# Performance work log

Hardware: AMD Instinct MI355X
Metric: run time of the kernel (lower is better)

Reference implementation:

```python
import jax, jax.numpy as jnp
import numpy as np

B, P, NOBJ = 16, 19248, 32
NUM_CLASSES = 81  # 80 foreground + background (code uses num_classes+1 w/o focal loss)
POS_TH, NEG_TH = 0.5, 0.4
VAR0, VAR1 = 0.1, 0.2  # standard SSD encode variances
NEGPOS_RATIO = 3


def setup_inputs() -> dict:
    key = jax.random.key(0)
    k1, k2, k3, k4, k5 = jax.random.split(key, 5)
    loc_data = jax.random.normal(k1, (B, P, 4), jnp.float32)
    conf_data = jax.random.normal(k2, (B, P, NUM_CLASSES), jnp.float32)
    # priors in (cx, cy, w, h), normalized coords
    pc = jax.random.uniform(k3, (P, 2), jnp.float32, 0.05, 0.95)
    pw = jax.random.uniform(jax.random.fold_in(k3, 1), (P, 2), jnp.float32, 0.05, 0.4)
    priors = jnp.concatenate([pc, pw], -1)
    # gt boxes in point form (xmin, ymin, xmax, ymax)
    gc = jax.random.uniform(k4, (B, NOBJ, 2), jnp.float32, 0.2, 0.8)
    gw = jax.random.uniform(jax.random.fold_in(k4, 1), (B, NOBJ, 2), jnp.float32, 0.05, 0.3)
    gt_boxes = jnp.concatenate([gc - gw / 2, gc + gw / 2], -1)
    gt_labels = jax.random.randint(k5, (B, NOBJ), 0, NUM_CLASSES - 1)  # 0..79
    return {"loc_data": loc_data, "conf_data": conf_data, "priors": priors,
            "gt_boxes": gt_boxes, "gt_labels": gt_labels}


def _point_form(p):
    # (cx,cy,w,h) -> (xmin,ymin,xmax,ymax)
    return jnp.concatenate([p[..., :2] - p[..., 2:] / 2, p[..., :2] + p[..., 2:] / 2], -1)


def _jaccard(a, b):
    # a: [N,4], b: [P,4] point form -> IoU [N,P]
    lt = jnp.maximum(a[:, None, :2], b[None, :, :2])
    rb = jnp.minimum(a[:, None, 2:], b[None, :, 2:])
    wh = jnp.clip(rb - lt, 0.0)
    inter = wh[..., 0] * wh[..., 1]
    area_a = (a[:, 2] - a[:, 0]) * (a[:, 3] - a[:, 1])
    area_b = (b[:, 2] - b[:, 0]) * (b[:, 3] - b[:, 1])
    return inter / (area_a[:, None] + area_b[None, :] - inter)


def _match_one(gt, labels, priors_pf, priors):
    # SSD match: per-prior best gt + force each gt's best prior to be positive
    ov = _jaccard(gt, priors_pf)                 # [N,P]
    best_prior_idx = jnp.argmax(ov, axis=1)      # [N]
    best_truth_ov = jnp.max(ov, axis=0)          # [P]
    best_truth_idx = jnp.argmax(ov, axis=0)      # [P]
    best_truth_ov = best_truth_ov.at[best_prior_idx].set(2.0)
    best_truth_idx = best_truth_idx.at[best_prior_idx].set(jnp.arange(gt.shape[0]))
    matched = gt[best_truth_idx]                 # [P,4] point form
    conf = labels[best_truth_idx] + 1
    conf = jnp.where(best_truth_ov < POS_TH, -1, conf)   # neutral band
    conf = jnp.where(best_truth_ov < NEG_TH, 0, conf)    # background
    # encode offsets with variances
    m_cxcy = (matched[:, :2] + matched[:, 2:]) / 2
    m_wh = matched[:, 2:] - matched[:, :2]
    g_cxcy = (m_cxcy - priors[:, :2]) / (VAR0 * priors[:, 2:])
    g_wh = jnp.log(m_wh / priors[:, 2:]) / VAR1
    return jnp.concatenate([g_cxcy, g_wh], -1), conf


def reference(loc_data, conf_data, priors, gt_boxes, gt_labels):
    priors_pf = _point_form(priors)
    loc_t, conf_t = jax.vmap(lambda g, l: _match_one(g, l, priors_pf, priors))(gt_boxes, gt_labels)
    loc_t = jax.lax.stop_gradient(loc_t)
    pos = conf_t > 0                                   # [B,P]
    n_pos = pos.sum(axis=1)                            # [B]
    N = jnp.maximum(pos.sum(), 1).astype(loc_data.dtype)
    # localization: smooth L1 over positives
    d = loc_data - loc_t
    ad = jnp.abs(d)
    sl1 = jnp.where(ad < 1.0, 0.5 * d * d, ad - 0.5)
    loss_l = jnp.sum(sl1 * pos[..., None])
    # confidence: hard negative mining at 3:1
    logp = jax.nn.log_softmax(conf_data, axis=-1)      # [B,P,C]
    ct = jnp.maximum(conf_t, 0)
    nll = -jnp.take_along_axis(logp, ct[..., None], axis=-1)[..., 0]  # [B,P]
    mine = jnp.where(pos | (conf_t < 0), 0.0, nll)     # exclude pos & neutral from mining
    rank = jnp.argsort(jnp.argsort(-mine, axis=1), axis=1)
    num_neg = jnp.minimum(NEGPOS_RATIO * n_pos, P - 1)
    neg = (rank < num_neg[:, None]) & (conf_t == 0)
    loss_c = jnp.sum(nll * (pos | neg))
    return jnp.stack([loss_l, loss_c]) / N
```

## Files before the change

### kernel.cpp

```cpp
#include <hip/hip_runtime.h>
#include <cstdint>
#include <cstddef>

#define BB 16
#define PP 19248
#define NOBJ 32
#define NCLS 81
#define POS_TH 0.5f
#define NEG_TH 0.4f
#define VAR0 0.1f
#define VAR1 0.2f
#define NEGPOS 3

#define MTB 256
#define NMB ((PP + MTB - 1) / MTB)
#define MAINB 1024
#define ROWS_PB 64
#define NSLOT ((PP + ROWS_PB - 1) / ROWS_PB)
#define ST 1024

#define HSHIFT 19
#define HSIZE 8192
#define HPT (HSIZE / ST)
#define CAP HSIZE

__global__ __launch_bounds__(MTB) void k_match(const float* __restrict__ priors,
                                               const float* __restrict__ gt_boxes,
                                               unsigned long long* __restrict__ gkey,
                                               float* __restrict__ bto,
                                               int* __restrict__ bti) {
    const int b = blockIdx.y;
    const int p = blockIdx.x * MTB + threadIdx.x;
    const int wid = threadIdx.x >> 6, lane = threadIdx.x & 63;
    __shared__ float4 sg[NOBJ];
    __shared__ unsigned long long wkey[4][NOBJ];
    if (threadIdx.x < NOBJ) sg[threadIdx.x] = ((const float4*)gt_boxes)[b * NOBJ + threadIdx.x];
    __syncthreads();

    const bool valid = p < PP;
    float px1 = 0.f, py1 = 0.f, px2 = 0.f, py2 = 0.f, parea = 0.f;
    if (valid) {
        float4 pr = ((const float4*)priors)[p];
        float hw = pr.z / 2.0f, hh = pr.w / 2.0f;
        px1 = pr.x - hw; py1 = pr.y - hh; px2 = pr.x + hw; py2 = pr.y + hh;
        parea = (px2 - px1) * (py2 - py1);
    }

    float best = -1.0f;
    int bn = 0;
    for (int n = 0; n < NOBJ; ++n) {
        float4 g = sg[n];
        float iou = -1.0f;
        if (valid) {
            {
#pragma clang fp contract(off)
                float ix1 = fmaxf(g.x, px1), iy1 = fmaxf(g.y, py1);
                float ix2 = fminf(g.z, px2), iy2 = fminf(g.w, py2);
                float iw = fmaxf(ix2 - ix1, 0.0f), ih = fmaxf(iy2 - iy1, 0.0f);
                float inter = iw * ih;
                float garea = (g.z - g.x) * (g.w - g.y);
                iou = inter / (garea + parea - inter);
            }
        }
        if (iou > best) { best = iou; bn = n; }

        float m = iou;
        m = fmaxf(m, __shfl_xor(m, 1, 64));
        m = fmaxf(m, __shfl_xor(m, 2, 64));
        m = fmaxf(m, __shfl_xor(m, 4, 64));
        m = fmaxf(m, __shfl_xor(m, 8, 64));
        m = fmaxf(m, __shfl_xor(m, 16, 64));
        m = fmaxf(m, __shfl_xor(m, 32, 64));
        unsigned long long ball = __ballot(iou == m);
        if (lane == 0) {
            unsigned long long key = 0ull;
            if (m >= 0.0f) {
                unsigned psrc = (unsigned)(blockIdx.x * MTB + wid * 64 +
                                           (int)__builtin_ctzll(ball));
                key = (((unsigned long long)__float_as_uint(m)) << 32) |
                      (unsigned long long)(0xFFFFFFFFu - psrc);
            }
            wkey[wid][n] = key;
        }
    }

    if (valid) {
        bto[(size_t)b * PP + p] = best;
        bti[(size_t)b * PP + p] = bn;
    }
    __syncthreads();
    if (threadIdx.x < NOBJ) {
        unsigned long long k0 = wkey[0][threadIdx.x];
        unsigned long long k1 = wkey[1][threadIdx.x];
        unsigned long long k2 = wkey[2][threadIdx.x];
        unsigned long long k3 = wkey[3][threadIdx.x];
        if (k1 > k0) k0 = k1;
        if (k2 > k0) k0 = k2;
        if (k3 > k0) k0 = k3;
        atomicMax(&gkey[b * NOBJ + threadIdx.x], k0);
    }
}

__device__ __forceinline__ float sl1(float d) {
    float ad = fabsf(d);
    return ad < 1.0f ? 0.5f * d * d : ad - 0.5f;
}

__global__ __launch_bounds__(MAINB, 8) void k_main(const float* __restrict__ loc_data,
                                                   const float* __restrict__ conf_data,
                                                   const float* __restrict__ priors,
                                                   const float* __restrict__ gt_boxes,
                                                   const int* __restrict__ gt_labels,
                                                   const float* __restrict__ bto,
                                                   const int* __restrict__ bti,
                                                   const unsigned long long* __restrict__ gkey,
                                                   float* __restrict__ mine,
                                                   float* __restrict__ p_ll,
                                                   float* __restrict__ p_lc,
                                                   int* __restrict__ p_np) {
    const int b = blockIdx.y;
    const int t = threadIdx.x;
    const int wid = t >> 6;
    const int lane = t & 63;
    const int g = lane >> 4;
    const int j = lane & 15;
    const int rbase = blockIdx.x * ROWS_PB + wid * 4;
    const int r = rbase + g;
    const bool valid = r < PP;

    unsigned pst = 0xFFFFFFFFu;
    if (lane < NOBJ) {
        unsigned long long key = gkey[b * NOBJ + lane];
        pst = 0xFFFFFFFFu - (unsigned)(key & 0xFFFFFFFFull);
    }

    const float* rowp = conf_data + ((size_t)b * PP + r) * NCLS;
    float s = 0.0f;
    if (valid) {
        s  = __expf(rowp[j]);
        s += __expf(rowp[j + 16]);
        s += __expf(rowp[j + 32]);
        s += __expf(rowp[j + 48]);
        s += __expf(rowp[j + 64]);
        if (j == 0) s += __expf(rowp[80]);
    }
    s += __shfl_xor(s, 1, 64);
    s += __shfl_xor(s, 2, 64);
    s += __shfl_xor(s, 4, 64);
    s += __shfl_xor(s, 8, 64);
    const float lse = __logf(s);

    unsigned long long b0 = __ballot(pst == (unsigned)(rbase + 0));
    unsigned long long b1 = __ballot(pst == (unsigned)(rbase + 1));
    unsigned long long b2 = __ballot(pst == (unsigned)(rbase + 2));
    unsigned long long b3 = __ballot(pst == (unsigned)(rbase + 3));
    unsigned long long mball = (g == 0) ? b0 : (g == 1) ? b1 : (g == 2) ? b2 : b3;

    float my_ll = 0.0f, my_lc = 0.0f;
    int my_pos = 0;

    if (valid && j == 0) {
        const size_t idx = (size_t)b * PP + r;
        float ov = bto[idx];
        int ti = bti[idx];
        if (mball) { ov = 2.0f; ti = 63 - __builtin_clzll(mball); }
        int conf_c = gt_labels[b * NOBJ + ti] + 1;
        if (ov < POS_TH) conf_c = -1;
        if (ov < NEG_TH) conf_c = 0;
        const int ct = conf_c > 0 ? conf_c : 0;
        const float nll = lse - rowp[ct];

        if (conf_c > 0) {
            my_pos = 1;
            my_lc = nll;
            float4 gbox = ((const float4*)gt_boxes)[b * NOBJ + ti];
            float4 pr = ((const float4*)priors)[r];
            float mcx = (gbox.x + gbox.z) / 2.0f, mcy = (gbox.y + gbox.w) / 2.0f;
            float mw = gbox.z - gbox.x, mh = gbox.w - gbox.y;
            float t0 = (mcx - pr.x) / (VAR0 * pr.z);
            float t1 = (mcy - pr.y) / (VAR0 * pr.w);
            float t2 = logf(mw / pr.z) / VAR1;
            float t3 = logf(mh / pr.w) / VAR1;
            float4 ld = ((const float4*)loc_data)[(size_t)b * PP + r];
            my_ll = sl1(ld.x - t0) + sl1(ld.y - t1) + sl1(ld.z - t2) + sl1(ld.w - t3);
        }
        mine[idx] = (conf_c == 0) ? nll : 0.0f;
    }

    for (int off = 32; off > 0; off >>= 1) {
        my_ll += __shfl_down(my_ll, off, 64);
        my_lc += __shfl_down(my_lc, off, 64);
        my_pos += __shfl_down(my_pos, off, 64);
    }
    __shared__ float rll[16], rlc[16];
    __shared__ int rnp[16];
    if (lane == 0) { rll[wid] = my_ll; rlc[wid] = my_lc; rnp[wid] = my_pos; }
    __syncthreads();
    if (t == 0) {
        float a = 0.0f, c = 0.0f;
        int n = 0;
#pragma unroll
        for (int w = 0; w < 16; ++w) { a += rll[w]; c += rlc[w]; n += rnp[w]; }
        p_ll[b * NSLOT + blockIdx.x] = a;
        p_lc[b * NSLOT + blockIdx.x] = c;
        p_np[b * NSLOT + blockIdx.x] = n;
    }
}

__global__ __launch_bounds__(ST) void k_select(const float* __restrict__ mine,
                                               const float* __restrict__ p_ll,
                                               const float* __restrict__ p_lc,
                                               const int* __restrict__ p_np,
                                               float* __restrict__ acc,
                                               int* __restrict__ acc_np,
                                               unsigned* __restrict__ done,
                                               float* __restrict__ out) {
    const int b = blockIdx.x;
    const int tid = threadIdx.x;
    const int wid = tid >> 6, lane = tid & 63;
    constexpr int NW = ST / 64;

    __shared__ unsigned hist[HSIZE];
    __shared__ unsigned s_tsum[ST];
    __shared__ unsigned s_wsum[NW];
    __shared__ float rll[NW], rlc[NW];
    __shared__ int rnp[NW];
    __shared__ float rs1[NW], rs2[NW];
    __shared__ unsigned rc2[NW];
    __shared__ float s_ll, s_lc, s_neg;
    __shared__ int s_np, s_B, s_G1;
    __shared__ unsigned s_cntB, s_cnt, s_prefix;
    __shared__ int s_rem;
    __shared__ unsigned h16[16];
    __shared__ unsigned swh[NW * 16];
    __shared__ unsigned stot[16];

    float ll = 0.0f, lc = 0.0f;
    int np = 0;
    for (int i = tid; i < NSLOT; i += ST) {
        ll += p_ll[b * NSLOT + i];
        lc += p_lc[b * NSLOT + i];
        np += p_np[b * NSLOT + i];
    }
    for (int off = 32; off > 0; off >>= 1) {
        ll += __shfl_down(ll, off, 64);
        lc += __shfl_down(lc, off, 64);
        np += __shfl_down(np, off, 64);
    }
    if (lane == 0) { rll[wid] = ll; rlc[wid] = lc; rnp[wid] = np; }
    __syncthreads();
    if (tid == 0) {
        float a = 0.0f, c = 0.0f;
        int n = 0;
        for (int w = 0; w < NW; ++w) { a += rll[w]; c += rlc[w]; n += rnp[w]; }
        s_ll = a; s_lc = c; s_np = n;
        s_neg = 0.0f;
    }
    __syncthreads();
    const int np_b = s_np;
    const int k = min(NEGPOS * np_b, PP - 1);

    const float* mv = mine + (size_t)b * PP;
    const float4* mv4 = (const float4*)mv;
    constexpr int PP4 = PP / 4;

    if (k > 0) {
        for (int i = tid; i < HSIZE; i += ST) hist[i] = 0u;
        __syncthreads();
        for (int i = tid; i < PP4; i += ST) {
            float4 v = mv4[i];
            atomicAdd(&hist[__float_as_uint(v.x) >> HSHIFT], 1u);
            atomicAdd(&hist[__float_as_uint(v.y) >> HSHIFT], 1u);
            atomicAdd(&hist[__float_as_uint(v.z) >> HSHIFT], 1u);
            atomicAdd(&hist[__float_as_uint(v.w) >> HSHIFT], 1u);
        }
        __syncthreads();

        unsigned tsum = 0;
        const int hb = tid * HPT;
#pragma unroll
        for (int v = 0; v < HPT; ++v) tsum += hist[hb + v];
        s_tsum[tid] = tsum;
        unsigned wsum = tsum;
        for (int off = 32; off > 0; off >>= 1) wsum += __shfl_down(wsum, off, 64);
        if (lane == 0) s_wsum[wid] = wsum;
        __syncthreads();
        if (tid == 0) {
            unsigned cum = 0;
            int w = NW - 1;
            for (; w > 0; --w) {
                if (cum + s_wsum[w] >= (unsigned)k) break;
                cum += s_wsum[w];
            }
            int t = (w + 1) * 64 - 1;
            for (; t > w * 64; --t) {
                if (cum + s_tsum[t] >= (unsigned)k) break;
                cum += s_tsum[t];
            }
            int bin = t * HPT + HPT - 1;
            for (; bin > t * HPT; --bin) {
                if (cum + hist[bin] >= (unsigned)k) break;
                cum += hist[bin];
            }
            s_B = bin;
            s_G1 = (int)cum;
            s_cntB = hist[bin];
            s_cnt = 0u;
        }
        __syncthreads();
        const int B = s_B;
        const int r = k - s_G1;
        const unsigned cntB = s_cntB;
        const unsigned bin_lo = (unsigned)B << HSHIFT;
        const unsigned hi_base = (unsigned)(B + 1) << HSHIFT;
        unsigned* cbuf = hist;

        if (cntB <= CAP) {
            float S1 = 0.0f;
            for (int i = tid; i < PP4; i += ST) {
                float4 v = mv4[i];
                unsigned bx = __float_as_uint(v.x);
                unsigned by = __float_as_uint(v.y);
                unsigned bz = __float_as_uint(v.z);
                unsigned bw = __float_as_uint(v.w);
                if (bx >= hi_base) S1 += v.x;
                else if (bx >= bin_lo) cbuf[atomicAdd(&s_cnt, 1u)] = bx;
                if (by >= hi_base) S1 += v.y;
                else if (by >= bin_lo) cbuf[atomicAdd(&s_cnt, 1u)] = by;
                if (bz >= hi_base) S1 += v.z;
                else if (bz >= bin_lo) cbuf[atomicAdd(&s_cnt, 1u)] = bz;
                if (bw >= hi_base) S1 += v.w;
                else if (bw >= bin_lo) cbuf[atomicAdd(&s_cnt, 1u)] = bw;
            }
            for (int off = 32; off > 0; off >>= 1) S1 += __shfl_down(S1, off, 64);
            if (lane == 0) rs1[wid] = S1;
            __syncthreads();

            if (tid == 0) { s_prefix = bin_lo; s_rem = r; }
            __syncthreads();
            for (int pass = 0; pass < 5; ++pass) {
                const int shift = (pass < 4) ? (15 - 4 * pass) : 0;
                const int width = (pass < 4) ? 4 : 3;
                const int nb = 1 << width;
                const unsigned hm = 0xFFFFFFFFu << (shift + width);
                if (tid < 16) h16[tid] = 0u;
                __syncthreads();
                const unsigned prefix = s_prefix;
                for (unsigned i = tid; i < cntB; i += ST) {
                    unsigned bits = cbuf[i];
                    if ((bits & hm) == prefix)
                        atomicAdd(&h16[(bits >> shift) & (nb - 1)], 1u);
                }
                __syncthreads();
                if (tid == 0) {
                    int rem = s_rem;
                    unsigned cum = 0;
                    int chosen = 0;
                    for (int v = nb - 1; v >= 0; --v) {
                        unsigned c = h16[v];
                        if (cum + c >= (unsigned)rem) { chosen = v; s_rem = rem - (int)cum; break; }
                        cum += c;
                    }
                    s_prefix = prefix | ((unsigned)chosen << shift);
                }
                __syncthreads();
            }
            const unsigned T = s_prefix;

            float S2 = 0.0f;
            unsigned c2 = 0;
            for (unsigned i = tid; i < cntB; i += ST) {
                unsigned bits = cbuf[i];
                if (bits > T) { S2 += __uint_as_float(bits); c2++; }
            }
            for (int off = 32; off > 0; off >>= 1) {
                S2 += __shfl_down(S2, off, 64);
                c2 += __shfl_down(c2, off, 64);
            }
            if (lane == 0) { rs2[wid] = S2; rc2[wid] = c2; }
            __syncthreads();
            if (tid == 0) {
                float S1t = 0.0f, S2t = 0.0f;
                unsigned c2t = 0;
                for (int w = 0; w < NW; ++w) { S1t += rs1[w]; S2t += rs2[w]; c2t += rc2[w]; }
                s_neg = S1t + S2t + (float)(r - (int)c2t) * __uint_as_float(T);
            }
            __syncthreads();
        } else {
            if (tid == 0) { s_prefix = 0u; s_rem = k; }
            __syncthreads();
            for (int pass = 0; pass < 8; ++pass) {
                const int shift = 28 - 4 * pass;
                const unsigned hm = (pass == 0) ? 0u : (0xFFFFFFFFu << (shift + 4));
                const unsigned prefix = s_prefix;
                unsigned cnt[16];
#pragma unroll
                for (int v = 0; v < 16; ++v) cnt[v] = 0u;
                for (int i = tid; i < PP; i += ST) {
                    unsigned bits = __float_as_uint(mv[i]);
                    unsigned key = ((bits & hm) == prefix) ? ((bits >> shift) & 15u) : 16u;
                    if (__any(key != 16u)) {
#pragma unroll
                        for (int v = 0; v < 16; ++v)
                            cnt[v] += (unsigned)__popcll(__ballot(key == (unsigned)v));
                    }
                }
                if (lane == 0) {
#pragma unroll
                    for (int v = 0; v < 16; ++v) swh[wid * 16 + v] = cnt[v];
                }
                __syncthreads();
                if (tid < 16) {
                    unsigned tt = 0;
#pragma unroll
                    for (int w = 0; w < NW; ++w) tt += swh[w * 16 + tid];
                    stot[tid] = tt;
                }
                __syncthreads();
                if (tid == 0) {
                    int rem = s_rem;
                    unsigned cum = 0;
                    int chosen = 0;
                    for (int v = 15; v >= 0; --v) {
                        unsigned c = stot[v];
                        if (cum + c >= (unsigned)rem) { chosen = v; s_rem = rem - (int)cum; break; }
                        cum += c;
                    }
                    s_prefix = prefix | ((unsigned)chosen << shift);
                }
                __syncthreads();
            }
            const unsigned T = s_prefix;
            float sum = 0.0f;
            unsigned cnt = 0;
            for (int i = tid; i < PP; i += ST) {
                float v = mv[i];
                if (__float_as_uint(v) > T) { sum += v; cnt++; }
            }
            for (int off = 32; off > 0; off >>= 1) {
                sum += __shfl_down(sum, off, 64);
                cnt += __shfl_down(cnt, off, 64);
            }
            if (lane == 0) { rs2[wid] = sum; rc2[wid] = cnt; }
            __syncthreads();
            if (tid == 0) {
                float S = 0.0f;
                int G = 0;
                for (int w = 0; w < NW; ++w) { S += rs2[w]; G += (int)rc2[w]; }
                s_neg = S + (float)(k - G) * __uint_as_float(T);
            }
            __syncthreads();
        }
    }

    if (tid == 0) {
        atomicAdd(&acc[0], s_ll);
        atomicAdd(&acc[1], s_lc + s_neg);
        atomicAdd(acc_np, np_b);
        __threadfence();
        unsigned prev = atomicAdd(done, 1u);
        if (prev == BB - 1) {
            int tp = atomicAdd(acc_np, 0);
            float N = (float)max(tp, 1);
            float a0 = atomicAdd(&acc[0], 0.0f);
            float a1 = atomicAdd(&acc[1], 0.0f);
            out[0] = a0 / N;
            out[1] = a1 / N;
        }
    }
}

extern "C" void kernel_launch(void* const* d_in, const int* in_sizes, int n_in,
                              void* d_out, int out_size, void* d_ws, size_t ws_size,
                              hipStream_t stream) {
    const float* loc    = (const float*)d_in[0];
    const float* conf   = (const float*)d_in[1];
    const float* priors = (const float*)d_in[2];
    const float* gt     = (const float*)d_in[3];
    const int*   labels = (const int*)d_in[4];
    float* out = (float*)d_out;

    char* ws = (char*)d_ws;
    const size_t SZ_BP = (size_t)BB * PP * 4;
    const size_t SZ_SLOT = (size_t)BB * NSLOT * 4;
    unsigned long long* gkey = (unsigned long long*)ws;
    float*    acc    = (float*)   (ws + 4096);
    int*      acc_np = (int*)     (ws + 4104);
    unsigned* done   = (unsigned*)(ws + 4108);
    float* bto  = (float*)(ws + 4224);
    int*   bti  = (int*)  (ws + 4224 + SZ_BP);
    float* mine = (float*)(ws + 4224 + 2 * SZ_BP);
    float* p_ll = (float*)(ws + 4224 + 3 * SZ_BP);
    float* p_lc = (float*)(ws + 4224 + 3 * SZ_BP + SZ_SLOT);
    int*   p_np = (int*)  (ws + 4224 + 3 * SZ_BP + 2 * SZ_SLOT);

    (void)hipMemsetAsync(ws, 0, 4224, stream);

    dim3 mg(NMB, BB);
    k_match<<<mg, MTB, 0, stream>>>(priors, gt, gkey, bto, bti);

    dim3 kg(NSLOT, BB);
    k_main<<<kg, MAINB, 0, stream>>>(loc, conf, priors, gt, labels, bto, bti, gkey,
                                     mine, p_ll, p_lc, p_np);

    k_select<<<BB, ST, 0, stream>>>(mine, p_ll, p_lc, p_np, acc, acc_np, done, out);
}
```

Before: 211.8 us.

## Recompute per-prior best-truth IoU in main kernel instead of storing it

The match kernel no longer writes the per-prior best overlap and index arrays. The main kernel recomputes them instead: each 16-lane group evaluates the IoU of its prior against 32 ground-truth boxes, two per lane, then takes an argmax across lanes that breaks ties toward the lower index. This removes a round trip of two B×P global arrays and issues the conf loads before the IoU math so their latency can be hidden. The cost is extra ALU work and register pressure in the main kernel.

```diff
diff --git a/kernel.cpp b/kernel.cpp
--- a/kernel.cpp
+++ b/kernel.cpp
@@ -26,9 +26,7 @@
 
 __global__ __launch_bounds__(MTB) void k_match(const float* __restrict__ priors,
                                                const float* __restrict__ gt_boxes,
-                                               unsigned long long* __restrict__ gkey,
-                                               float* __restrict__ bto,
-                                               int* __restrict__ bti) {
+                                               unsigned long long* __restrict__ gkey) {
     const int b = blockIdx.y;
     const int p = blockIdx.x * MTB + threadIdx.x;
     const int wid = threadIdx.x >> 6, lane = threadIdx.x & 63;
@@ -46,8 +44,6 @@
         parea = (px2 - px1) * (py2 - py1);
     }
 
-    float best = -1.0f;
-    int bn = 0;
     for (int n = 0; n < NOBJ; ++n) {
         float4 g = sg[n];
         float iou = -1.0f;
@@ -62,7 +58,6 @@
                 iou = inter / (garea + parea - inter);
             }
         }
-        if (iou > best) { best = iou; bn = n; }
 
         float m = iou;
         m = fmaxf(m, __shfl_xor(m, 1, 64));
@@ -84,10 +79,6 @@
         }
     }
 
-    if (valid) {
-        bto[(size_t)b * PP + p] = best;
-        bti[(size_t)b * PP + p] = bn;
-    }
     __syncthreads();
     if (threadIdx.x < NOBJ) {
         unsigned long long k0 = wkey[0][threadIdx.x];
@@ -111,8 +102,6 @@
                                                    const float* __restrict__ priors,
                                                    const float* __restrict__ gt_boxes,
                                                    const int* __restrict__ gt_labels,
-                                                   const float* __restrict__ bto,
-                                                   const int* __restrict__ bti,
                                                    const unsigned long long* __restrict__ gkey,
                                                    float* __restrict__ mine,
                                                    float* __restrict__ p_ll,
@@ -135,15 +124,53 @@
     }
 
     const float* rowp = conf_data + ((size_t)b * PP + r) * NCLS;
-    float s = 0.0f;
+    float c0 = 0.f, c1 = 0.f, c2 = 0.f, c3 = 0.f, c4 = 0.f, c80 = 0.f;
+    float4 pr = make_float4(0.f, 0.f, 0.f, 0.f);
     if (valid) {
-        s  = __expf(rowp[j]);
-        s += __expf(rowp[j + 16]);
-        s += __expf(rowp[j + 32]);
-        s += __expf(rowp[j + 48]);
-        s += __expf(rowp[j + 64]);
-        if (j == 0) s += __expf(rowp[80]);
-    }
+        c0 = rowp[j];
+        c1 = rowp[j + 16];
+        c2 = rowp[j + 32];
+        c3 = rowp[j + 48];
+        c4 = rowp[j + 64];
+        if (j == 0) c80 = rowp[80];
+        pr = ((const float4*)priors)[r];
+    }
+    float4 ga = ((const float4*)gt_boxes)[b * NOBJ + j];
+    float4 gb = ((const float4*)gt_boxes)[b * NOBJ + j + 16];
+    float bov;
+    int bidx;
+    {
+#pragma clang fp contract(off)
+        float hw = pr.z / 2.0f, hh = pr.w / 2.0f;
+        float px1 = pr.x - hw, py1 = pr.y - hh, px2 = pr.x + hw, py2 = pr.y + hh;
+        float parea = (px2 - px1) * (py2 - py1);
+
+        float ix1 = fmaxf(ga.x, px1), iy1 = fmaxf(ga.y, py1);
+        float ix2 = fminf(ga.z, px2), iy2 = fminf(ga.w, py2);
+        float iw = fmaxf(ix2 - ix1, 0.0f), ih = fmaxf(iy2 - iy1, 0.0f);
+        float inter = iw * ih;
+        float garea = (ga.z - ga.x) * (ga.w - ga.y);
+        float iouA = inter / (garea + parea - inter);
+
+        ix1 = fmaxf(gb.x, px1); iy1 = fmaxf(gb.y, py1);
+        ix2 = fminf(gb.z, px2); iy2 = fminf(gb.w, py2);
+        iw = fmaxf(ix2 - ix1, 0.0f); ih = fmaxf(iy2 - iy1, 0.0f);
+        inter = iw * ih;
+        garea = (gb.z - gb.x) * (gb.w - gb.y);
+        float iouB = inter / (garea + parea - inter);
+
+        bov = iouA; bidx = j;
+        if (iouB > bov) { bov = iouB; bidx = j + 16; }
+    }
+#pragma unroll
+    for (int m = 1; m < 16; m <<= 1) {
+        float o = __shfl_xor(bov, m, 64);
+        int oi = __shfl_xor(bidx, m, 64);
+        if (o > bov || (o == bov && oi < bidx)) { bov = o; bidx = oi; }
+    }
+
+    float s = __expf(c0) + __expf(c1) + __expf(c2) + __expf(c3) + __expf(c4);
+    if (j == 0) s += __expf(c80);
     s += __shfl_xor(s, 1, 64);
     s += __shfl_xor(s, 2, 64);
     s += __shfl_xor(s, 4, 64);
@@ -161,8 +188,8 @@
 
     if (valid && j == 0) {
         const size_t idx = (size_t)b * PP + r;
-        float ov = bto[idx];
-        int ti = bti[idx];
+        float ov = bov;
+        int ti = bidx;
         if (mball) { ov = 2.0f; ti = 63 - __builtin_clzll(mball); }
         int conf_c = gt_labels[b * NOBJ + ti] + 1;
         if (ov < POS_TH) conf_c = -1;
@@ -174,7 +201,6 @@
             my_pos = 1;
             my_lc = nll;
             float4 gbox = ((const float4*)gt_boxes)[b * NOBJ + ti];
-            float4 pr = ((const float4*)priors)[r];
             float mcx = (gbox.x + gbox.z) / 2.0f, mcy = (gbox.y + gbox.w) / 2.0f;
             float mw = gbox.z - gbox.x, mh = gbox.w - gbox.y;
             float t0 = (mcx - pr.x) / (VAR0 * pr.z);
@@ -487,20 +513,18 @@
     float*    acc    = (float*)   (ws + 4096);
     int*      acc_np = (int*)     (ws + 4104);
     unsigned* done   = (unsigned*)(ws + 4108);
-    float* bto  = (float*)(ws + 4224);
-    int*   bti  = (int*)  (ws + 4224 + SZ_BP);
-    float* mine = (float*)(ws + 4224 + 2 * SZ_BP);
-    float* p_ll = (float*)(ws + 4224 + 3 * SZ_BP);
-    float* p_lc = (float*)(ws + 4224 + 3 * SZ_BP + SZ_SLOT);
-    int*   p_np = (int*)  (ws + 4224 + 3 * SZ_BP + 2 * SZ_SLOT);
+    float* mine = (float*)(ws + 4224);
+    float* p_ll = (float*)(ws + 4224 + SZ_BP);
+    float* p_lc = (float*)(ws + 4224 + SZ_BP + SZ_SLOT);
+    int*   p_np = (int*)  (ws + 4224 + SZ_BP + 2 * SZ_SLOT);
 
     (void)hipMemsetAsync(ws, 0, 4224, stream);
 
     dim3 mg(NMB, BB);
-    k_match<<<mg, MTB, 0, stream>>>(priors, gt, gkey, bto, bti);
+    k_match<<<mg, MTB, 0, stream>>>(priors, gt, gkey);
 
     dim3 kg(NSLOT, BB);
-    k_main<<<kg, MAINB, 0, stream>>>(loc, conf, priors, gt, labels, bto, bti, gkey,
+    k_main<<<kg, MAINB, 0, stream>>>(loc, conf, priors, gt, labels, gkey,
                                      mine, p_ll, p_lc, p_np);
 
     k_select<<<BB, ST, 0, stream>>>(mine, p_ll, p_lc, p_np, acc, acc_np, done, out);
```

Result: slower. 217.2 us (+2.6%).
